# Performance work log

Hardware: AMD Instinct MI355X
Metric: run time of the kernel (lower is better)

## Reference

```python
import jax, jax.numpy as jnp
import numpy as np


def setup_inputs() -> dict:
    key = jax.random.key(0)
    k1, k2, k3 = jax.random.split(key, 3)
    N, C, Nf, W, H = 8, 256, 16, 28, 28
    l = jax.random.normal(k1, (N, C, Nf, W, H), dtype=jnp.float32)
    g = jax.random.normal(k2, (N, C, 1, 1, 1), dtype=jnp.float32)
    # 1x1x1 Conv3d(in=C, out=1, bias=False) weight collapses to a length-C vector
    w = jax.random.normal(k3, (C,), dtype=jnp.float32) * (1.0 / np.sqrt(C))
    return {"l": l, "g": g, "w": w}


def reference(l, g, w):
    # l: [N,C,Nf,W,H], g broadcastable to l, w: [C]
    N, C, Nf, W, H = l.shape
    # compatibility score: channel dot-product (1x1x1 conv, out_channels=1)
    c = jnp.einsum('ncfwh,c->nfwh', l + g, w)                      # [N,Nf,W,H]
    # softmax over the spatial dims (W*H) per frame, normalize_attn=True
    a = jax.nn.softmax(c.reshape(N, Nf, W * H), axis=-1)           # [N,Nf,WH]
    a = a.reshape(N, Nf, W, H)
    # attention-weighted spatial sum pooling -> [N,C,Nf]
    g_out = jnp.einsum('nfwh,ncfwh->ncf', a, l)
    # module returns raw compatibility map (pre-softmax) squeezed, and pooled g
    return (c, g_out)
```

## Files before the change

### kernel.cpp

```cpp
#include <hip/hip_runtime.h>
#include <math.h>

constexpr int N_ = 8, C_ = 256, F_ = 16, WH_ = 784;
constexpr int CH_STRIDE = F_ * WH_;
constexpr int COUT_SZ = N_ * F_ * WH_;

__device__ inline float wave_reduce_sum(float v) {
#pragma unroll
  for (int o = 32; o > 0; o >>= 1) v += __shfl_down(v, o, 64);
  return v;
}
__device__ inline float wave_reduce_max(float v) {
#pragma unroll
  for (int o = 32; o > 0; o >>= 1) v = fmaxf(v, __shfl_down(v, o, 64));
  return v;
}

__global__ __launch_bounds__(1024) void mfla_kernel(
    const float* __restrict__ l, const float* __restrict__ g,
    const float* __restrict__ w, float* __restrict__ out) {
  __shared__ float w_s[C_];
  __shared__ float e_s[WH_];
  __shared__ float red_s[16];
  __shared__ float bc_s;

  const int b = blockIdx.x;
  const int n = b >> 4;
  const int f = b & 15;
  const int tid = threadIdx.x;
  const int lane = tid & 63;
  const int wv = tid >> 6;

  if (tid < C_) w_s[tid] = w[tid];

  float gv = (tid < C_) ? g[n * C_ + tid] * w[tid] : 0.f;
  gv = wave_reduce_sum(gv);
  if (lane == 0) red_s[wv] = gv;
  __syncthreads();
  if (tid == 0) {
    float s = 0.f;
#pragma unroll
    for (int i = 0; i < 16; ++i) s += red_s[i];
    bc_s = s;
  }
  __syncthreads();
  const float gb = bc_s;

  const size_t base_nf = (size_t)(n * C_ * F_ + f) * WH_;
  float cv = -3.4e38f;
  if (tid < WH_) {
    const float* lp = l + base_nf + tid;
    float acc = 0.f;
#pragma unroll 8
    for (int c = 0; c < C_; ++c) acc = fmaf(lp[(size_t)c * CH_STRIDE], w_s[c], acc);
    cv = acc + gb;
    out[b * WH_ + tid] = cv;
  }

  float m = wave_reduce_max(cv);
  __syncthreads();
  if (lane == 0) red_s[wv] = m;
  __syncthreads();
  if (tid == 0) {
    float mm = red_s[0];
#pragma unroll
    for (int i = 1; i < 16; ++i) mm = fmaxf(mm, red_s[i]);
    bc_s = mm;
  }
  __syncthreads();
  const float cmax = bc_s;

  float e = 0.f;
  if (tid < WH_) {
    e = expf(cv - cmax);
    e_s[tid] = e;
  }
  float s = wave_reduce_sum(e);
  __syncthreads();
  if (lane == 0) red_s[wv] = s;
  __syncthreads();
  if (tid == 0) {
    float ss = 0.f;
#pragma unroll
    for (int i = 0; i < 16; ++i) ss += red_s[i];
    bc_s = 1.f / ss;
  }
  __syncthreads();
  const float inv_sum = bc_s;

  const int p0 = lane << 2;
  const float4 ew0 = *reinterpret_cast<const float4*>(&e_s[p0]);
  const float4 ew1 = *reinterpret_cast<const float4*>(&e_s[p0 + 256]);
  const float4 ew2 = *reinterpret_cast<const float4*>(&e_s[p0 + 512]);
  float4 ew3 = make_float4(0.f, 0.f, 0.f, 0.f);
  if (lane < 4) ew3 = *reinterpret_cast<const float4*>(&e_s[768 + p0]);

#pragma unroll 1
  for (int i = 0; i < 16; ++i) {
    const int c = wv + (i << 4);
    const float* bp = l + ((size_t)(n * C_ + c) * F_ + f) * WH_;
    float4 lv0 = *reinterpret_cast<const float4*>(bp + p0);
    float4 lv1 = *reinterpret_cast<const float4*>(bp + p0 + 256);
    float4 lv2 = *reinterpret_cast<const float4*>(bp + p0 + 512);
    float4 lv3 = make_float4(0.f, 0.f, 0.f, 0.f);
    if (lane < 4) lv3 = *reinterpret_cast<const float4*>(bp + 768 + p0);

    float acc = 0.f;
    acc = fmaf(lv0.x, ew0.x, acc); acc = fmaf(lv0.y, ew0.y, acc);
    acc = fmaf(lv0.z, ew0.z, acc); acc = fmaf(lv0.w, ew0.w, acc);
    acc = fmaf(lv1.x, ew1.x, acc); acc = fmaf(lv1.y, ew1.y, acc);
    acc = fmaf(lv1.z, ew1.z, acc); acc = fmaf(lv1.w, ew1.w, acc);
    acc = fmaf(lv2.x, ew2.x, acc); acc = fmaf(lv2.y, ew2.y, acc);
    acc = fmaf(lv2.z, ew2.z, acc); acc = fmaf(lv2.w, ew2.w, acc);
    acc = fmaf(lv3.x, ew3.x, acc); acc = fmaf(lv3.y, ew3.y, acc);
    acc = fmaf(lv3.z, ew3.z, acc); acc = fmaf(lv3.w, ew3.w, acc);

    acc = wave_reduce_sum(acc);
    if (lane == 0)
      out[COUT_SZ + (size_t)(n * C_ + c) * F_ + f] = acc * inv_sum;
  }
}

extern "C" void kernel_launch(void* const* d_in, const int* in_sizes, int n_in,
                              void* d_out, int out_size, void* d_ws, size_t ws_size,
                              hipStream_t stream) {
  const float* l = (const float*)d_in[0];
  const float* g = (const float*)d_in[1];
  const float* w = (const float*)d_in[2];
  float* out = (float*)d_out;
  mfla_kernel<<<dim3(N_ * F_), dim3(1024), 0, stream>>>(l, g, w, out);
}
```

Measured before the change: 166.7 us.

## Split fused kernel into score and pooling kernels with more parallel blocks

The single fused kernel (one block per (n,f), 128 blocks) is split into a score kernel and a pooling kernel, each launched with 256 blocks. The score kernel splits the channel dimension across 8 thread groups, uses float4 loads with a shared-memory reduction, and splits the spatial dimension in half. The pooling kernel reads the scores back from the output buffer and splits channels in half across blocks. The aim is to fill more of the GPU's compute units and raise memory-level parallelism, at the cost of a second launch and reading l twice, though the two passes over l could be served from cache in both designs.

```diff
diff --git a/kernel.cpp b/kernel.cpp
--- a/kernel.cpp
+++ b/kernel.cpp
@@ -16,49 +16,88 @@
   return v;
 }
 
-__global__ __launch_bounds__(1024) void mfla_kernel(
+__global__ __launch_bounds__(1024) void c_kernel(
     const float* __restrict__ l, const float* __restrict__ g,
     const float* __restrict__ w, float* __restrict__ out) {
   __shared__ float w_s[C_];
-  __shared__ float e_s[WH_];
   __shared__ float red_s[16];
-  __shared__ float bc_s;
+  __shared__ float gb_s;
+  __shared__ float4 ps[8][98];
 
-  const int b = blockIdx.x;
-  const int n = b >> 4;
-  const int f = b & 15;
+  const int bid = blockIdx.x;
+  const int nf = bid >> 1;
+  const int ph = bid & 1;
+  const int n = nf >> 4;
+  const int f = nf & 15;
   const int tid = threadIdx.x;
-  const int lane = tid & 63;
-  const int wv = tid >> 6;
+  const int q = tid >> 7;
+  const int p4 = tid & 127;
 
   if (tid < C_) w_s[tid] = w[tid];
 
   float gv = (tid < C_) ? g[n * C_ + tid] * w[tid] : 0.f;
   gv = wave_reduce_sum(gv);
-  if (lane == 0) red_s[wv] = gv;
+  if ((tid & 63) == 0) red_s[tid >> 6] = gv;
   __syncthreads();
   if (tid == 0) {
     float s = 0.f;
 #pragma unroll
     for (int i = 0; i < 16; ++i) s += red_s[i];
-    bc_s = s;
+    gb_s = s;
   }
   __syncthreads();
-  const float gb = bc_s;
 
-  const size_t base_nf = (size_t)(n * C_ * F_ + f) * WH_;
+  if (p4 < 98) {
+    const float* lp = l + ((size_t)(n * C_ + (q << 5)) * F_ + f) * WH_ +
+                      ph * 392 + (p4 << 2);
+    float4 acc = make_float4(0.f, 0.f, 0.f, 0.f);
+#pragma unroll 8
+    for (int c = 0; c < 32; ++c) {
+      const float4 lv =
+          *reinterpret_cast<const float4*>(lp + (size_t)c * CH_STRIDE);
+      const float wc = w_s[(q << 5) + c];
+      acc.x = fmaf(lv.x, wc, acc.x);
+      acc.y = fmaf(lv.y, wc, acc.y);
+      acc.z = fmaf(lv.z, wc, acc.z);
+      acc.w = fmaf(lv.w, wc, acc.w);
+    }
+    ps[q][p4] = acc;
+  }
+  __syncthreads();
+
+  if (tid < 98) {
+    float4 s = ps[0][tid];
+#pragma unroll
+    for (int i = 1; i < 8; ++i) {
+      const float4 t = ps[i][tid];
+      s.x += t.x; s.y += t.y; s.z += t.z; s.w += t.w;
+    }
+    const float gb = gb_s;
+    s.x += gb; s.y += gb; s.z += gb; s.w += gb;
+    *reinterpret_cast<float4*>(
+        &out[(size_t)nf * WH_ + ph * 392 + (tid << 2)]) = s;
+  }
+}
+
+__global__ __launch_bounds__(1024) void pool_kernel(
+    const float* __restrict__ l, float* __restrict__ out) {
+  __shared__ float e_s[WH_];
+  __shared__ float red_s[16];
+  __shared__ float bc_s;
+
+  const int bid = blockIdx.x;
+  const int nf = bid >> 1;
+  const int ch = bid & 1;
+  const int n = nf >> 4;
+  const int f = nf & 15;
+  const int tid = threadIdx.x;
+  const int lane = tid & 63;
+  const int wv = tid >> 6;
+
   float cv = -3.4e38f;
-  if (tid < WH_) {
-    const float* lp = l + base_nf + tid;
-    float acc = 0.f;
-#pragma unroll 8
-    for (int c = 0; c < C_; ++c) acc = fmaf(lp[(size_t)c * CH_STRIDE], w_s[c], acc);
-    cv = acc + gb;
-    out[b * WH_ + tid] = cv;
-  }
+  if (tid < WH_) cv = out[(size_t)nf * WH_ + tid];
 
   float m = wave_reduce_max(cv);
-  __syncthreads();
   if (lane == 0) red_s[wv] = m;
   __syncthreads();
   if (tid == 0) {
@@ -96,8 +135,8 @@
   if (lane < 4) ew3 = *reinterpret_cast<const float4*>(&e_s[768 + p0]);
 
 #pragma unroll 1
-  for (int i = 0; i < 16; ++i) {
-    const int c = wv + (i << 4);
+  for (int i = 0; i < 8; ++i) {
+    const int c = (ch << 7) + wv + (i << 4);
     const float* bp = l + ((size_t)(n * C_ + c) * F_ + f) * WH_;
     float4 lv0 = *reinterpret_cast<const float4*>(bp + p0);
     float4 lv1 = *reinterpret_cast<const float4*>(bp + p0 + 256);
@@ -122,11 +161,12 @@
 }
 
 extern "C" void kernel_launch(void* const* d_in, const int* in_sizes, int n_in,
-                              void* d_out, int out_size, void* d_ws, size_t ws_size,
-                              hipStream_t stream) {
+                              void* d_out, int out_size, void* d_ws,
+                              size_t ws_size, hipStream_t stream) {
   const float* l = (const float*)d_in[0];
   const float* g = (const float*)d_in[1];
   const float* w = (const float*)d_in[2];
   float* out = (float*)d_out;
-  mfla_kernel<<<dim3(N_ * F_), dim3(1024), 0, stream>>>(l, g, w, out);
+  c_kernel<<<dim3(2 * N_ * F_), dim3(1024), 0, stream>>>(l, g, w, out);
+  pool_kernel<<<dim3(2 * N_ * F_), dim3(1024), 0, stream>>>(l, out);
 }
```

Measured after the change: 166.2 us. Within noise of the previous version (-0.3%).

## Stage spatial tiles in LDS, split each frame across two blocks, combine partial sums

Applied to the files above, without the earlier changes.

Each (n,f) frame is split across two blocks. Each block streams its 392 spatial positions in 56-wide tiles through shared memory with register prefetch, so l is read from global memory once instead of twice. The softmax now uses an unshifted exp with no max subtraction, which lets the partial weighted sums and exp totals be finished by a small second combine kernel. This doubles the block count for more parallelism and removes the second pass over l. In exchange it adds a kernel launch and workspace traffic, and large scores could overflow exp.

```diff
diff --git a/kernel.cpp b/kernel.cpp
--- a/kernel.cpp
+++ b/kernel.cpp
@@ -4,35 +4,35 @@
 constexpr int N_ = 8, C_ = 256, F_ = 16, WH_ = 784;
 constexpr int CH_STRIDE = F_ * WH_;
 constexpr int COUT_SZ = N_ * F_ * WH_;
+constexpr int TILE = 56;
+constexpr int NT = 7;
+constexpr int LSTR = 60;
+constexpr int F4PT = TILE / 4;
+constexpr int STAGE_TOT = C_ * F4PT;
 
 __device__ inline float wave_reduce_sum(float v) {
 #pragma unroll
   for (int o = 32; o > 0; o >>= 1) v += __shfl_down(v, o, 64);
   return v;
 }
-__device__ inline float wave_reduce_max(float v) {
-#pragma unroll
-  for (int o = 32; o > 0; o >>= 1) v = fmaxf(v, __shfl_down(v, o, 64));
-  return v;
-}
 
-__global__ __launch_bounds__(1024) void mfla_kernel(
+__global__ __launch_bounds__(1024) void fused_kernel(
     const float* __restrict__ l, const float* __restrict__ g,
-    const float* __restrict__ w, float* __restrict__ out) {
+    const float* __restrict__ w, float* __restrict__ out,
+    float* __restrict__ ws) {
+  __shared__ float buf[C_ * LSTR];
   __shared__ float w_s[C_];
-  __shared__ float e_s[WH_];
+  __shared__ float e_s[TILE];
   __shared__ float red_s[16];
-  __shared__ float bc_s;
+  __shared__ float gb_s;
 
-  const int b = blockIdx.x;
-  const int n = b >> 4;
-  const int f = b & 15;
+  const int bid = blockIdx.x;
+  const int nf = bid >> 1, ph = bid & 1;
+  const int n = nf >> 4, f = nf & 15;
   const int tid = threadIdx.x;
-  const int lane = tid & 63;
-  const int wv = tid >> 6;
+  const int lane = tid & 63, wv = tid >> 6;
 
   if (tid < C_) w_s[tid] = w[tid];
-
   float gv = (tid < C_) ? g[n * C_ + tid] * w[tid] : 0.f;
   gv = wave_reduce_sum(gv);
   if (lane == 0) red_s[wv] = gv;
@@ -41,92 +41,110 @@
     float s = 0.f;
 #pragma unroll
     for (int i = 0; i < 16; ++i) s += red_s[i];
-    bc_s = s;
+    gb_s = s;
   }
   __syncthreads();
-  const float gb = bc_s;
+  const float gb = gb_s;
 
-  const size_t base_nf = (size_t)(n * C_ * F_ + f) * WH_;
-  float cv = -3.4e38f;
-  if (tid < WH_) {
-    const float* lp = l + base_nf + tid;
-    float acc = 0.f;
-#pragma unroll 8
-    for (int c = 0; c < C_; ++c) acc = fmaf(lp[(size_t)c * CH_STRIDE], w_s[c], acc);
-    cv = acc + gb;
-    out[b * WH_ + tid] = cv;
+  int offG[4], offL[4];
+  bool act[4];
+#pragma unroll
+  for (int k = 0; k < 4; ++k) {
+    const int idx = k * 1024 + tid;
+    act[k] = (k < 3) || (tid < 512);
+    const int c = act[k] ? (idx / F4PT) : 0;
+    const int j = idx - c * F4PT;
+    offG[k] = c * CH_STRIDE + (j << 2);
+    offL[k] = c * LSTR + (j << 2);
+  }
+  const size_t gbase =
+      (size_t)n * (C_ * CH_STRIDE) + (size_t)f * WH_ + ph * 392;
+
+  float4 st[4];
+#pragma unroll
+  for (int k = 0; k < 4; ++k)
+    if (act[k]) st[k] = *reinterpret_cast<const float4*>(l + gbase + offG[k]);
+
+  float gacc = 0.f;
+  float s_part = 0.f;
+  const int gc = tid >> 2, q = tid & 3;
+  const int p = tid >> 3, s8 = tid & 7;
+
+  for (int t = 0; t < NT; ++t) {
+#pragma unroll
+    for (int k = 0; k < 4; ++k)
+      if (act[k]) *reinterpret_cast<float4*>(&buf[offL[k]]) = st[k];
+    __syncthreads();
+
+    if (t + 1 < NT) {
+      const float* lp = l + gbase + (t + 1) * TILE;
+#pragma unroll
+      for (int k = 0; k < 4; ++k)
+        if (act[k]) st[k] = *reinterpret_cast<const float4*>(lp + offG[k]);
+    }
+
+    if (tid < TILE * 8) {
+      float acc = 0.f;
+#pragma unroll
+      for (int k = 0; k < 32; ++k) {
+        const int c = s8 + (k << 3);
+        acc = fmaf(buf[c * LSTR + p], w_s[c], acc);
+      }
+      acc += __shfl_down(acc, 4, 64);
+      acc += __shfl_down(acc, 2, 64);
+      acc += __shfl_down(acc, 1, 64);
+      if (s8 == 0) {
+        const float cp = acc + gb;
+        out[nf * WH_ + ph * 392 + t * TILE + p] = cp;
+        const float e = __expf(cp);
+        e_s[p] = e;
+        s_part += e;
+      }
+    }
+    __syncthreads();
+
+    {
+      const int pb = q * F4PT;
+#pragma unroll
+      for (int j = 0; j < 14; ++j)
+        gacc = fmaf(buf[gc * LSTR + pb + j], e_s[pb + j], gacc);
+    }
+    __syncthreads();
   }
 
-  float m = wave_reduce_max(cv);
-  __syncthreads();
-  if (lane == 0) red_s[wv] = m;
+  gacc += __shfl_down(gacc, 2, 64);
+  gacc += __shfl_down(gacc, 1, 64);
+  if (q == 0) ws[bid * C_ + gc] = gacc;
+
+  float sp = wave_reduce_sum(s_part);
+  if (lane == 0) red_s[wv] = sp;
   __syncthreads();
   if (tid == 0) {
-    float mm = red_s[0];
+    float ssum = 0.f;
 #pragma unroll
-    for (int i = 1; i < 16; ++i) mm = fmaxf(mm, red_s[i]);
-    bc_s = mm;
-  }
-  __syncthreads();
-  const float cmax = bc_s;
-
-  float e = 0.f;
-  if (tid < WH_) {
-    e = expf(cv - cmax);
-    e_s[tid] = e;
-  }
-  float s = wave_reduce_sum(e);
-  __syncthreads();
-  if (lane == 0) red_s[wv] = s;
-  __syncthreads();
-  if (tid == 0) {
-    float ss = 0.f;
-#pragma unroll
-    for (int i = 0; i < 16; ++i) ss += red_s[i];
-    bc_s = 1.f / ss;
-  }
-  __syncthreads();
-  const float inv_sum = bc_s;
-
-  const int p0 = lane << 2;
-  const float4 ew0 = *reinterpret_cast<const float4*>(&e_s[p0]);
-  const float4 ew1 = *reinterpret_cast<const float4*>(&e_s[p0 + 256]);
-  const float4 ew2 = *reinterpret_cast<const float4*>(&e_s[p0 + 512]);
-  float4 ew3 = make_float4(0.f, 0.f, 0.f, 0.f);
-  if (lane < 4) ew3 = *reinterpret_cast<const float4*>(&e_s[768 + p0]);
-
-#pragma unroll 1
-  for (int i = 0; i < 16; ++i) {
-    const int c = wv + (i << 4);
-    const float* bp = l + ((size_t)(n * C_ + c) * F_ + f) * WH_;
-    float4 lv0 = *reinterpret_cast<const float4*>(bp + p0);
-    float4 lv1 = *reinterpret_cast<const float4*>(bp + p0 + 256);
-    float4 lv2 = *reinterpret_cast<const float4*>(bp + p0 + 512);
-    float4 lv3 = make_float4(0.f, 0.f, 0.f, 0.f);
-    if (lane < 4) lv3 = *reinterpret_cast<const float4*>(bp + 768 + p0);
-
-    float acc = 0.f;
-    acc = fmaf(lv0.x, ew0.x, acc); acc = fmaf(lv0.y, ew0.y, acc);
-    acc = fmaf(lv0.z, ew0.z, acc); acc = fmaf(lv0.w, ew0.w, acc);
-    acc = fmaf(lv1.x, ew1.x, acc); acc = fmaf(lv1.y, ew1.y, acc);
-    acc = fmaf(lv1.z, ew1.z, acc); acc = fmaf(lv1.w, ew1.w, acc);
-    acc = fmaf(lv2.x, ew2.x, acc); acc = fmaf(lv2.y, ew2.y, acc);
-    acc = fmaf(lv2.z, ew2.z, acc); acc = fmaf(lv2.w, ew2.w, acc);
-    acc = fmaf(lv3.x, ew3.x, acc); acc = fmaf(lv3.y, ew3.y, acc);
-    acc = fmaf(lv3.z, ew3.z, acc); acc = fmaf(lv3.w, ew3.w, acc);
-
-    acc = wave_reduce_sum(acc);
-    if (lane == 0)
-      out[COUT_SZ + (size_t)(n * C_ + c) * F_ + f] = acc * inv_sum;
+    for (int i = 0; i < 16; ++i) ssum += red_s[i];
+    ws[65536 + bid] = ssum;
   }
 }
 
+__global__ __launch_bounds__(1024) void combine_kernel(
+    float* __restrict__ out, const float* __restrict__ ws) {
+  const int tg = blockIdx.x * 1024 + threadIdx.x;
+  const int nf = tg >> 8, c = tg & 255;
+  const int n = nf >> 4, f = nf & 15;
+  const float G = ws[(2 * nf) * C_ + c] + ws[(2 * nf + 1) * C_ + c];
+  const float S = ws[65536 + 2 * nf] + ws[65536 + 2 * nf + 1];
+  out[COUT_SZ + (size_t)(n * C_ + c) * F_ + f] = G / S;
+}
+
 extern "C" void kernel_launch(void* const* d_in, const int* in_sizes, int n_in,
-                              void* d_out, int out_size, void* d_ws, size_t ws_size,
-                              hipStream_t stream) {
+                              void* d_out, int out_size, void* d_ws,
+                              size_t ws_size, hipStream_t stream) {
   const float* l = (const float*)d_in[0];
   const float* g = (const float*)d_in[1];
   const float* w = (const float*)d_in[2];
   float* out = (float*)d_out;
-  mfla_kernel<<<dim3(N_ * F_), dim3(1024), 0, stream>>>(l, g, w, out);
+  float* ws = (float*)d_ws;
+  fused_kernel<<<dim3(2 * N_ * F_), dim3(1024), 0, stream>>>(l, g, w, out, ws);
+  combine_kernel<<<dim3(32), dim3(1024), 0, stream>>>(out, ws);
 }
```

Result: slower. 179.3 us (+7.5%).
